# Kernel optimization log

Hardware: AMD Instinct MI355X
Metric: run time of the kernel (lower is better)

The kernel has to match this reference:

```python
import jax, jax.numpy as jnp
import numpy as np

B, H, S, DK = 2, 16, 2048, 64
NEG = -1000000000.0

def setup_inputs() -> dict:
    key = jax.random.key(0)
    k1, k2, k3, k4 = jax.random.split(key, 4)
    Q = jax.random.normal(k1, (B, H, S, DK), dtype=jnp.float32)
    K = jax.random.normal(k2, (B, H, S, DK), dtype=jnp.float32)
    V = jax.random.normal(k3, (B, H, S, DK), dtype=jnp.float32)
    mask = jax.random.randint(k4, (B, 1, S, S), 0, 2).astype(bool)
    return {"Q": Q, "K": K, "V": V, "mask": mask}

def reference(Q, K, V, mask):
    sqrt_dk = jnp.asarray(DK ** 0.5, Q.dtype)
    # [B,H,S,S] scores, materialized as in the original module
    score = jnp.einsum('bhqd,bhkd->bhqk', Q, K) / sqrt_dk
    score = jnp.where(mask, jnp.asarray(NEG, score.dtype), score)
    attn_prob = jax.nn.softmax(score, axis=-1)  # dropout p=0.0 -> identity
    context = jnp.einsum('bhqk,bhkd->bhqd', attn_prob, V)
    return (context, attn_prob)
```

## Files before the change

kernel.cpp:

```cpp
#include <hip/hip_runtime.h>

static constexpr int Bc  = 2;
static constexpr int Hc  = 16;
static constexpr int Sc  = 2048;
static constexpr int DKc = 64;
static constexpr float SC2  = 0.18033688011112043f;

typedef __attribute__((ext_vector_type(8)))  short short8v;
typedef __attribute__((ext_vector_type(16))) float f32x16;
typedef __attribute__((ext_vector_type(4)))  float f32x4;

__device__ __forceinline__ unsigned short f2bf(float f) {
    union { float f; unsigned u; } v; v.f = f;
    unsigned r = v.u + 0x7FFFu + ((v.u >> 16) & 1u);
    return (unsigned short)(r >> 16);
}
__device__ __forceinline__ unsigned cvtpk(float lo, float hi) {
    unsigned r;
    asm("v_cvt_pk_bf16_f32 %0, %1, %2" : "=v"(r) : "v"(lo), "v"(hi));
    return r;
}
__device__ __forceinline__ float fexp2(float x) {
    float r;
    asm("v_exp_f32 %0, %1" : "=v"(r) : "v"(x));
    return r;
}

__global__ void kfrag_kernel(const float* __restrict__ K, unsigned short* __restrict__ Kf) {
    int i = blockIdx.x * 256 + threadIdx.x;
    int lane = i & 63, ks = (i >> 6) & 3, t = (i >> 8) & 63, bh = i >> 14;
    int hi = lane >> 5, l31 = lane & 31;
    const float* src = K + (((size_t)bh * Sc + t * 32 + l31) * DKc + ks * 16 + hi * 8);
    float4 a = *(const float4*)src;
    float4 c = *(const float4*)(src + 4);
    short8v s;
    s[0]=(short)f2bf(a.x); s[1]=(short)f2bf(a.y); s[2]=(short)f2bf(a.z); s[3]=(short)f2bf(a.w);
    s[4]=(short)f2bf(c.x); s[5]=(short)f2bf(c.y); s[6]=(short)f2bf(c.z); s[7]=(short)f2bf(c.w);
    *(short8v*)&Kf[(size_t)i * 8] = s;
}

__global__ void vfrag_kernel(const float* __restrict__ V, unsigned short* __restrict__ Vf) {
    int i = blockIdx.x * 256 + threadIdx.x;
    int lane = i & 63, dblk = (i >> 6) & 1, ks = (i >> 7) & 1, t = (i >> 8) & 63, bh = i >> 14;
    int hi = lane >> 5, l31 = lane & 31;
    int k0 = t * 32 + ks * 16 + hi * 8, d = dblk * 32 + l31;
    const float* vb = V + ((size_t)bh * Sc + k0) * DKc + d;
    short8v s;
    #pragma unroll
    for (int u = 0; u < 8; ++u) s[u] = (short)f2bf(vb[(size_t)u * DKc]);
    *(short8v*)&Vf[(size_t)i * 8] = s;
}

__global__ void mfrag_kernel(const int* __restrict__ M, unsigned* __restrict__ Mf) {
    int w = blockIdx.x * 4 + (threadIdx.x >> 6);
    int lane = threadIdx.x & 63;
    const int* row = M + (size_t)w * Sc;
    int b = w >> 11, q = w & 2047, qt = q >> 5, r = q & 31;
    unsigned* ob = Mf + (size_t)(b * 64 + qt) * 2048 + r;
    for (int tp = 0; tp < 32; ++tp) {
        unsigned long long bal = __ballot(row[tp * 64 + lane] != 0);
        if (lane == 0)  ob[(size_t)(2 * tp)     * 32] = (unsigned)bal;
        if (lane == 32) ob[(size_t)(2 * tp + 1) * 32] = (unsigned)(bal >> 32);
    }
}

__global__ __launch_bounds__(256, 3)
void attn_ctx(const float* __restrict__ Q, const unsigned short* __restrict__ Kf,
              const unsigned short* __restrict__ Vf, const unsigned* __restrict__ Mf,
              float* __restrict__ Lb, float* __restrict__ out)
{
    const int wg  = (int)blockIdx.x;
    const int swz = (wg & 7) * 256 + (wg >> 3);
    const int bh  = swz >> 6;
    const int qt  = swz & 63;
    const int qb  = qt << 5;
    const int b   = bh >> 4;

    const int tid  = (int)threadIdx.x;
    const int wid  = tid >> 6;
    const int lane = tid & 63;
    const int hi   = lane >> 5;
    const int l31  = lane & 31;

    __shared__ float lbuf[4][32];
    __shared__ float lfin[32];
    __shared__ float pall[4096];

    const unsigned short* kfb = Kf + (size_t)bh * 131072;
    const unsigned short* vfb = Vf + (size_t)bh * 131072;
    const unsigned*       mfb = Mf + (size_t)(b * 64 + qt) * 2048;

    short8v qf[4];
    {
        const float* qrow = Q + ((size_t)bh * Sc + qb + l31) * DKc;
        #pragma unroll
        for (int ks = 0; ks < 4; ++ks) {
            const float* p0 = qrow + ks * 16 + hi * 8;
            float4 a = *(const float4*)p0;
            float4 c = *(const float4*)(p0 + 4);
            short8v f;
            f[0]=(short)f2bf(a.x); f[1]=(short)f2bf(a.y); f[2]=(short)f2bf(a.z); f[3]=(short)f2bf(a.w);
            f[4]=(short)f2bf(c.x); f[5]=(short)f2bf(c.y); f[6]=(short)f2bf(c.z); f[7]=(short)f2bf(c.w);
            qf[ks] = f;
        }
    }

    f32x16 acc0, acc1;
    #pragma unroll
    for (int u = 0; u < 16; ++u) { acc0[u] = 0.0f; acc1[u] = 0.0f; }
    float l_run = 0.0f;

    for (int i = 0; i < 16; ++i) {
        const int t = i * 4 + wid;
        short8v k4[4];
        #pragma unroll
        for (int ks = 0; ks < 4; ++ks)
            k4[ks] = *(const short8v*)&kfb[((size_t)(t * 4 + ks) * 64 + lane) * 8];
        short8v v4[4];
        #pragma unroll
        for (int u = 0; u < 4; ++u)
            v4[u] = *(const short8v*)&vfb[((size_t)(t * 4 + u) * 64 + lane) * 8];
        const unsigned mw = mfb[t * 32 + l31] >> (4 * hi);

        f32x16 sc;
        #pragma unroll
        for (int u = 0; u < 16; ++u) sc[u] = 0.0f;
        #pragma unroll
        for (int ks = 0; ks < 4; ++ks)
            sc = __builtin_amdgcn_mfma_f32_32x32x16_bf16(k4[ks], qf[ks], sc, 0, 0, 0);

        #pragma unroll
        for (int g = 0; g < 4; ++g)
            #pragma unroll
            for (int j = 0; j < 4; ++j) {
                float a = sc[4*g+j] * SC2;
                a = ((mw >> (8*g + j)) & 1u) ? -1e30f : a;
                sc[4*g+j] = fexp2(a);
            }

        float ps = 0.0f;
        #pragma unroll
        for (int u = 0; u < 16; ++u) ps += sc[u];
        ps += __shfl_xor(ps, 32);
        l_run += ps;

        unsigned pk[8];
        #pragma unroll
        for (int g = 0; g < 4; ++g) {
            pk[2*g]   = cvtpk(sc[4*g],   sc[4*g+1]);
            pk[2*g+1] = cvtpk(sc[4*g+2], sc[4*g+3]);
        }
        #pragma unroll
        for (int ks = 0; ks < 2; ++ks) {
            unsigned o0x = pk[4*ks], o0y = pk[4*ks+1], o1x = pk[4*ks+2], o1y = pk[4*ks+3];
            unsigned s0x = __shfl_xor(o0x, 32), s0y = __shfl_xor(o0y, 32);
            unsigned s1x = __shfl_xor(o1x, 32), s1y = __shfl_xor(o1y, 32);
            union { unsigned u[4]; short8v s; } pa;
            pa.u[0] = hi ? s1x : o0x;
            pa.u[1] = hi ? s1y : o0y;
            pa.u[2] = hi ? o1x : s0x;
            pa.u[3] = hi ? o1y : s0y;
            acc0 = __builtin_amdgcn_mfma_f32_32x32x16_bf16(pa.s, v4[2*ks+0], acc0, 0, 0, 0);
            acc1 = __builtin_amdgcn_mfma_f32_32x32x16_bf16(pa.s, v4[2*ks+1], acc1, 0, 0, 0);
        }
    }

    if (hi == 0) lbuf[wid][l31] = l_run;
    __syncthreads();
    if (tid < 32) {
        float l = lbuf[0][tid] + lbuf[1][tid] + lbuf[2][tid] + lbuf[3][tid];
        lfin[tid] = l;
        Lb[(size_t)(bh * 64 + qt) * 32 + tid] = -__log2f(l);
    }

    __syncthreads();
    if (wid >= 2) {
        #pragma unroll
        for (int g = 0; g < 4; ++g)
            #pragma unroll
            for (int j = 0; j < 4; ++j) {
                int row = 8*g + 4*hi + j;
                pall[(wid - 2) * 2048 + row * 64 + l31]      = acc0[4*g+j];
                pall[(wid - 2) * 2048 + row * 64 + l31 + 32] = acc1[4*g+j];
            }
    }
    __syncthreads();
    if (wid < 2) {
        #pragma unroll
        for (int g = 0; g < 4; ++g)
            #pragma unroll
            for (int j = 0; j < 4; ++j) {
                int row = 8*g + 4*hi + j;
                acc0[4*g+j] += pall[wid * 2048 + row * 64 + l31];
                acc1[4*g+j] += pall[wid * 2048 + row * 64 + l31 + 32];
            }
    }
    __syncthreads();
    if (wid == 1) {
        #pragma unroll
        for (int g = 0; g < 4; ++g)
            #pragma unroll
            for (int j = 0; j < 4; ++j) {
                int row = 8*g + 4*hi + j;
                pall[row * 64 + l31]      = acc0[4*g+j];
                pall[row * 64 + l31 + 32] = acc1[4*g+j];
            }
    }
    __syncthreads();
    if (wid == 0) {
        #pragma unroll
        for (int g = 0; g < 4; ++g)
            #pragma unroll
            for (int j = 0; j < 4; ++j) {
                int row = 8*g + 4*hi + j;
                float rinv = 1.0f / lfin[row];
                float o0 = (acc0[4*g+j] + pall[row * 64 + l31])      * rinv;
                float o1 = (acc1[4*g+j] + pall[row * 64 + l31 + 32]) * rinv;
                size_t off = ((size_t)bh * Sc + qb + row) * DKc + l31;
                out[off]      = o0;
                out[off + 32] = o1;
            }
    }
}

__global__ __launch_bounds__(256, 4)
void attn_pstore(const float* __restrict__ Q, const unsigned short* __restrict__ Kf,
                 const unsigned* __restrict__ Mf, const float* __restrict__ Lb,
                 float* __restrict__ out)
{
    const int wg  = (int)blockIdx.x;
    const int swz = (wg & 7) * 256 + (wg >> 3);
    const int bh  = swz >> 6;
    const int qt  = swz & 63;
    const int qb  = qt << 5;
    const int b   = bh >> 4;

    const int tid  = (int)threadIdx.x;
    const int wid  = tid >> 6;
    const int lane = tid & 63;
    const int hi   = lane >> 5;
    const int l31  = lane & 31;

    __shared__ char sbuf[32768];

    const unsigned short* kfb = Kf + (size_t)bh * 131072;
    const unsigned*       mfb = Mf + (size_t)(b * 64 + qt) * 2048;
    const float bl = Lb[(size_t)(bh * 64 + qt) * 32 + l31];

    short8v qf[4];
    {
        const float* qrow = Q + ((size_t)bh * Sc + qb + l31) * DKc;
        #pragma unroll
        for (int ks = 0; ks < 4; ++ks) {
            const float* p0 = qrow + ks * 16 + hi * 8;
            float4 a = *(const float4*)p0;
            float4 c = *(const float4*)(p0 + 4);
            short8v f;
            f[0]=(short)f2bf(a.x); f[1]=(short)f2bf(a.y); f[2]=(short)f2bf(a.z); f[3]=(short)f2bf(a.w);
            f[4]=(short)f2bf(c.x); f[5]=(short)f2bf(c.y); f[6]=(short)f2bf(c.z); f[7]=(short)f2bf(c.w);
            qf[ks] = f;
        }
    }

    float* prow0 = out + (size_t)Bc * Hc * Sc * DKc + ((size_t)bh * Sc + qb) * Sc;

    for (int r = 0; r < 8; ++r) {
        #pragma unroll
        for (int sub = 0; sub < 2; ++sub) {
            const int t = r * 8 + sub * 4 + wid;
            short8v k4[4];
            #pragma unroll
            for (int ks = 0; ks < 4; ++ks)
                k4[ks] = *(const short8v*)&kfb[((size_t)(t * 4 + ks) * 64 + lane) * 8];
            const unsigned mw = mfb[t * 32 + l31] >> (4 * hi);

            f32x16 sc;
            #pragma unroll
            for (int u = 0; u < 16; ++u) sc[u] = 0.0f;
            #pragma unroll
            for (int ks = 0; ks < 4; ++ks)
                sc = __builtin_amdgcn_mfma_f32_32x32x16_bf16(k4[ks], qf[ks], sc, 0, 0, 0);

            #pragma unroll
            for (int g = 0; g < 4; ++g)
                #pragma unroll
                for (int j = 0; j < 4; ++j) {
                    float a = sc[4*g+j] * SC2 + bl;
                    a = ((mw >> (8*g + j)) & 1u) ? -1e30f : a;
                    sc[4*g+j] = fexp2(a);
                }

            #pragma unroll
            for (int g = 0; g < 4; ++g) {
                f32x4 st; st.x = sc[4*g]; st.y = sc[4*g+1]; st.z = sc[4*g+2]; st.w = sc[4*g+3];
                *(f32x4*)(sbuf + l31 * 1024 +
                          ((sub * 512 + wid * 128 + 32*g + 16*hi) ^ ((l31 & 15) << 4))) = st;
            }
        }
        __syncthreads();
        #pragma unroll
        for (int j2 = 0; j2 < 8; ++j2) {
            const int row = j2 * 4 + wid;
            f32x4 ld = *(const f32x4*)(sbuf + row * 1024 +
                                       ((lane * 16) ^ ((row & 15) << 4)));
            __builtin_nontemporal_store(ld, (f32x4*)(prow0 + (size_t)row * Sc + r * 256 + lane * 4));
        }
        __syncthreads();
    }
}

extern "C" void kernel_launch(void* const* d_in, const int* in_sizes, int n_in,
                              void* d_out, int out_size, void* d_ws, size_t ws_size,
                              hipStream_t stream)
{
    const float* Q = (const float*)d_in[0];
    const float* K = (const float*)d_in[1];
    const float* V = (const float*)d_in[2];
    const int*   M = (const int*)d_in[3];
    float* out = (float*)d_out;

    unsigned short* Kf = (unsigned short*)d_ws;
    unsigned short* Vf = (unsigned short*)((char*)d_ws + (8u << 20));
    unsigned*       Mf = (unsigned*)((char*)d_ws + (16u << 20));
    float*          Lb = (float*)((char*)d_ws + (17u << 20));

    hipLaunchKernelGGL(kfrag_kernel, dim3(2048), dim3(256), 0, stream, K, Kf);
    hipLaunchKernelGGL(vfrag_kernel, dim3(2048), dim3(256), 0, stream, V, Vf);
    hipLaunchKernelGGL(mfrag_kernel, dim3(1024), dim3(256), 0, stream, M, Mf);
    hipLaunchKernelGGL(attn_ctx,     dim3(2048), dim3(256), 0, stream, Q, Kf, Vf, Mf, Lb, out);
    hipLaunchKernelGGL(attn_pstore,  dim3(2048), dim3(256), 0, stream, Q, Kf, Mf, Lb, out);
}
```

Measured before the change: 193.0 us.

## Move PV accumulation into probability-store pass using pre-normalized probabilities

The first pass now only computes the row sums of exp scores (log-sum), dropping the V loads and PV MFMAs. The second pass, which already produces normalized probabilities for the attention-prob output, now also multiplies them by V and reduces the context across waves through reused shared memory, so no final division is needed. This shortens the first pass and lets it run at higher occupancy, at the cost of more register pressure and extra V traffic in the store-bound second kernel.

```diff
diff --git a/kernel.cpp b/kernel.cpp
--- a/kernel.cpp
+++ b/kernel.cpp
@@ -64,10 +64,9 @@
     }
 }
 
-__global__ __launch_bounds__(256, 3)
-void attn_ctx(const float* __restrict__ Q, const unsigned short* __restrict__ Kf,
-              const unsigned short* __restrict__ Vf, const unsigned* __restrict__ Mf,
-              float* __restrict__ Lb, float* __restrict__ out)
+__global__ __launch_bounds__(256, 5)
+void attn_lsum(const float* __restrict__ Q, const unsigned short* __restrict__ Kf,
+               const unsigned* __restrict__ Mf, float* __restrict__ Lb)
 {
     const int wg  = (int)blockIdx.x;
     const int swz = (wg & 7) * 256 + (wg >> 3);
@@ -83,11 +82,8 @@
     const int l31  = lane & 31;
 
     __shared__ float lbuf[4][32];
-    __shared__ float lfin[32];
-    __shared__ float pall[4096];
 
     const unsigned short* kfb = Kf + (size_t)bh * 131072;
-    const unsigned short* vfb = Vf + (size_t)bh * 131072;
     const unsigned*       mfb = Mf + (size_t)(b * 64 + qt) * 2048;
 
     short8v qf[4];
@@ -105,21 +101,13 @@
         }
     }
 
-    f32x16 acc0, acc1;
-    #pragma unroll
-    for (int u = 0; u < 16; ++u) { acc0[u] = 0.0f; acc1[u] = 0.0f; }
     float l_run = 0.0f;
-
     for (int i = 0; i < 16; ++i) {
         const int t = i * 4 + wid;
         short8v k4[4];
         #pragma unroll
         for (int ks = 0; ks < 4; ++ks)
             k4[ks] = *(const short8v*)&kfb[((size_t)(t * 4 + ks) * 64 + lane) * 8];
-        short8v v4[4];
-        #pragma unroll
-        for (int u = 0; u < 4; ++u)
-            v4[u] = *(const short8v*)&vfb[((size_t)(t * 4 + u) * 64 + lane) * 8];
         const unsigned mw = mfb[t * 32 + l31] >> (4 * hi);
 
         f32x16 sc;
@@ -129,104 +117,30 @@
         for (int ks = 0; ks < 4; ++ks)
             sc = __builtin_amdgcn_mfma_f32_32x32x16_bf16(k4[ks], qf[ks], sc, 0, 0, 0);
 
+        float ps = 0.0f;
         #pragma unroll
         for (int g = 0; g < 4; ++g)
             #pragma unroll
             for (int j = 0; j < 4; ++j) {
                 float a = sc[4*g+j] * SC2;
                 a = ((mw >> (8*g + j)) & 1u) ? -1e30f : a;
-                sc[4*g+j] = fexp2(a);
-            }
-
-        float ps = 0.0f;
-        #pragma unroll
-        for (int u = 0; u < 16; ++u) ps += sc[u];
+                ps += fexp2(a);
+            }
         ps += __shfl_xor(ps, 32);
         l_run += ps;
-
-        unsigned pk[8];
-        #pragma unroll
-        for (int g = 0; g < 4; ++g) {
-            pk[2*g]   = cvtpk(sc[4*g],   sc[4*g+1]);
-            pk[2*g+1] = cvtpk(sc[4*g+2], sc[4*g+3]);
-        }
-        #pragma unroll
-        for (int ks = 0; ks < 2; ++ks) {
-            unsigned o0x = pk[4*ks], o0y = pk[4*ks+1], o1x = pk[4*ks+2], o1y = pk[4*ks+3];
-            unsigned s0x = __shfl_xor(o0x, 32), s0y = __shfl_xor(o0y, 32);
-            unsigned s1x = __shfl_xor(o1x, 32), s1y = __shfl_xor(o1y, 32);
-            union { unsigned u[4]; short8v s; } pa;
-            pa.u[0] = hi ? s1x : o0x;
-            pa.u[1] = hi ? s1y : o0y;
-            pa.u[2] = hi ? o1x : s0x;
-            pa.u[3] = hi ? o1y : s0y;
-            acc0 = __builtin_amdgcn_mfma_f32_32x32x16_bf16(pa.s, v4[2*ks+0], acc0, 0, 0, 0);
-            acc1 = __builtin_amdgcn_mfma_f32_32x32x16_bf16(pa.s, v4[2*ks+1], acc1, 0, 0, 0);
-        }
-    }
-
+    }
     if (hi == 0) lbuf[wid][l31] = l_run;
     __syncthreads();
     if (tid < 32) {
         float l = lbuf[0][tid] + lbuf[1][tid] + lbuf[2][tid] + lbuf[3][tid];
-        lfin[tid] = l;
         Lb[(size_t)(bh * 64 + qt) * 32 + tid] = -__log2f(l);
     }
-
-    __syncthreads();
-    if (wid >= 2) {
-        #pragma unroll
-        for (int g = 0; g < 4; ++g)
-            #pragma unroll
-            for (int j = 0; j < 4; ++j) {
-                int row = 8*g + 4*hi + j;
-                pall[(wid - 2) * 2048 + row * 64 + l31]      = acc0[4*g+j];
-                pall[(wid - 2) * 2048 + row * 64 + l31 + 32] = acc1[4*g+j];
-            }
-    }
-    __syncthreads();
-    if (wid < 2) {
-        #pragma unroll
-        for (int g = 0; g < 4; ++g)
-            #pragma unroll
-            for (int j = 0; j < 4; ++j) {
-                int row = 8*g + 4*hi + j;
-                acc0[4*g+j] += pall[wid * 2048 + row * 64 + l31];
-                acc1[4*g+j] += pall[wid * 2048 + row * 64 + l31 + 32];
-            }
-    }
-    __syncthreads();
-    if (wid == 1) {
-        #pragma unroll
-        for (int g = 0; g < 4; ++g)
-            #pragma unroll
-            for (int j = 0; j < 4; ++j) {
-                int row = 8*g + 4*hi + j;
-                pall[row * 64 + l31]      = acc0[4*g+j];
-                pall[row * 64 + l31 + 32] = acc1[4*g+j];
-            }
-    }
-    __syncthreads();
-    if (wid == 0) {
-        #pragma unroll
-        for (int g = 0; g < 4; ++g)
-            #pragma unroll
-            for (int j = 0; j < 4; ++j) {
-                int row = 8*g + 4*hi + j;
-                float rinv = 1.0f / lfin[row];
-                float o0 = (acc0[4*g+j] + pall[row * 64 + l31])      * rinv;
-                float o1 = (acc1[4*g+j] + pall[row * 64 + l31 + 32]) * rinv;
-                size_t off = ((size_t)bh * Sc + qb + row) * DKc + l31;
-                out[off]      = o0;
-                out[off + 32] = o1;
-            }
-    }
 }
 
 __global__ __launch_bounds__(256, 4)
-void attn_pstore(const float* __restrict__ Q, const unsigned short* __restrict__ Kf,
-                 const unsigned* __restrict__ Mf, const float* __restrict__ Lb,
-                 float* __restrict__ out)
+void attn_store_pv(const float* __restrict__ Q, const unsigned short* __restrict__ Kf,
+                   const unsigned short* __restrict__ Vf, const unsigned* __restrict__ Mf,
+                   const float* __restrict__ Lb, float* __restrict__ out)
 {
     const int wg  = (int)blockIdx.x;
     const int swz = (wg & 7) * 256 + (wg >> 3);
@@ -244,6 +158,7 @@
     __shared__ char sbuf[32768];
 
     const unsigned short* kfb = Kf + (size_t)bh * 131072;
+    const unsigned short* vfb = Vf + (size_t)bh * 131072;
     const unsigned*       mfb = Mf + (size_t)(b * 64 + qt) * 2048;
     const float bl = Lb[(size_t)(bh * 64 + qt) * 32 + l31];
 
@@ -262,7 +177,12 @@
         }
     }
 
+    float* ctx   = out;
     float* prow0 = out + (size_t)Bc * Hc * Sc * DKc + ((size_t)bh * Sc + qb) * Sc;
+
+    f32x16 acc0, acc1;
+    #pragma unroll
+    for (int u = 0; u < 16; ++u) { acc0[u] = 0.0f; acc1[u] = 0.0f; }
 
     for (int r = 0; r < 8; ++r) {
         #pragma unroll
@@ -272,6 +192,10 @@
             #pragma unroll
             for (int ks = 0; ks < 4; ++ks)
                 k4[ks] = *(const short8v*)&kfb[((size_t)(t * 4 + ks) * 64 + lane) * 8];
+            short8v v4[4];
+            #pragma unroll
+            for (int u = 0; u < 4; ++u)
+                v4[u] = *(const short8v*)&vfb[((size_t)(t * 4 + u) * 64 + lane) * 8];
             const unsigned mw = mfb[t * 32 + l31] >> (4 * hi);
 
             f32x16 sc;
@@ -296,6 +220,26 @@
                 *(f32x4*)(sbuf + l31 * 1024 +
                           ((sub * 512 + wid * 128 + 32*g + 16*hi) ^ ((l31 & 15) << 4))) = st;
             }
+
+            unsigned pk[8];
+            #pragma unroll
+            for (int g = 0; g < 4; ++g) {
+                pk[2*g]   = cvtpk(sc[4*g],   sc[4*g+1]);
+                pk[2*g+1] = cvtpk(sc[4*g+2], sc[4*g+3]);
+            }
+            #pragma unroll
+            for (int ks = 0; ks < 2; ++ks) {
+                unsigned o0x = pk[4*ks], o0y = pk[4*ks+1], o1x = pk[4*ks+2], o1y = pk[4*ks+3];
+                unsigned s0x = __shfl_xor(o0x, 32), s0y = __shfl_xor(o0y, 32);
+                unsigned s1x = __shfl_xor(o1x, 32), s1y = __shfl_xor(o1y, 32);
+                union { unsigned u[4]; short8v s; } pa;
+                pa.u[0] = hi ? s1x : o0x;
+                pa.u[1] = hi ? s1y : o0y;
+                pa.u[2] = hi ? o1x : s0x;
+                pa.u[3] = hi ? o1y : s0y;
+                acc0 = __builtin_amdgcn_mfma_f32_32x32x16_bf16(pa.s, v4[2*ks+0], acc0, 0, 0, 0);
+                acc1 = __builtin_amdgcn_mfma_f32_32x32x16_bf16(pa.s, v4[2*ks+1], acc1, 0, 0, 0);
+            }
         }
         __syncthreads();
         #pragma unroll
@@ -306,6 +250,54 @@
             __builtin_nontemporal_store(ld, (f32x4*)(prow0 + (size_t)row * Sc + r * 256 + lane * 4));
         }
         __syncthreads();
+    }
+
+    float* pall = (float*)sbuf;
+    if (wid >= 2) {
+        #pragma unroll
+        for (int g = 0; g < 4; ++g)
+            #pragma unroll
+            for (int j = 0; j < 4; ++j) {
+                int row = 8*g + 4*hi + j;
+                pall[(wid - 2) * 2048 + row * 64 + l31]      = acc0[4*g+j];
+                pall[(wid - 2) * 2048 + row * 64 + l31 + 32] = acc1[4*g+j];
+            }
+    }
+    __syncthreads();
+    if (wid < 2) {
+        #pragma unroll
+        for (int g = 0; g < 4; ++g)
+            #pragma unroll
+            for (int j = 0; j < 4; ++j) {
+                int row = 8*g + 4*hi + j;
+                acc0[4*g+j] += pall[wid * 2048 + row * 64 + l31];
+                acc1[4*g+j] += pall[wid * 2048 + row * 64 + l31 + 32];
+            }
+    }
+    __syncthreads();
+    if (wid == 1) {
+        #pragma unroll
+        for (int g = 0; g < 4; ++g)
+            #pragma unroll
+            for (int j = 0; j < 4; ++j) {
+                int row = 8*g + 4*hi + j;
+                pall[row * 64 + l31]      = acc0[4*g+j];
+                pall[row * 64 + l31 + 32] = acc1[4*g+j];
+            }
+    }
+    __syncthreads();
+    if (wid == 0) {
+        #pragma unroll
+        for (int g = 0; g < 4; ++g)
+            #pragma unroll
+            for (int j = 0; j < 4; ++j) {
+                int row = 8*g + 4*hi + j;
+                float o0 = acc0[4*g+j] + pall[row * 64 + l31];
+                float o1 = acc1[4*g+j] + pall[row * 64 + l31 + 32];
+                size_t off = ((size_t)bh * Sc + qb + row) * DKc + l31;
+                ctx[off]      = o0;
+                ctx[off + 32] = o1;
+            }
     }
 }
 
@@ -324,9 +316,9 @@
     unsigned*       Mf = (unsigned*)((char*)d_ws + (16u << 20));
     float*          Lb = (float*)((char*)d_ws + (17u << 20));
 
-    hipLaunchKernelGGL(kfrag_kernel, dim3(2048), dim3(256), 0, stream, K, Kf);
-    hipLaunchKernelGGL(vfrag_kernel, dim3(2048), dim3(256), 0, stream, V, Vf);
-    hipLaunchKernelGGL(mfrag_kernel, dim3(1024), dim3(256), 0, stream, M, Mf);
-    hipLaunchKernelGGL(attn_ctx,     dim3(2048), dim3(256), 0, stream, Q, Kf, Vf, Mf, Lb, out);
-    hipLaunchKernelGGL(attn_pstore,  dim3(2048), dim3(256), 0, stream, Q, Kf, Mf, Lb, out);
-}
+    hipLaunchKernelGGL(kfrag_kernel,  dim3(2048), dim3(256), 0, stream, K, Kf);
+    hipLaunchKernelGGL(vfrag_kernel,  dim3(2048), dim3(256), 0, stream, V, Vf);
+    hipLaunchKernelGGL(mfrag_kernel,  dim3(1024), dim3(256), 0, stream, M, Mf);
+    hipLaunchKernelGGL(attn_lsum,     dim3(2048), dim3(256), 0, stream, Q, Kf, Mf, Lb);
+    hipLaunchKernelGGL(attn_store_pv, dim3(2048), dim3(256), 0, stream, Q, Kf, Vf, Mf, Lb, out);
+}
```

Result: slower. 240.2 us (+24.5%).
